# Kernel tuning notes

Hardware: AMD Instinct MI355X
Metric: run time of the kernel (lower is better)

## Reference

```python
import jax, jax.numpy as jnp
import numpy as np

VOCAB = 100000
EMB = 300
HID = 128


def setup_inputs() -> dict:
    key = jax.random.key(0)
    ks = jax.random.split(key, 12)
    inp = {
        "query_terms": jax.random.randint(ks[0], (32,), 0, VOCAB),
        "feedback_docs": jax.random.randint(ks[1], (128, 1024), 0, VOCAB),
        "n_terms": 10,
        "embedding": jax.random.normal(ks[2], (VOCAB, EMB), dtype=jnp.float32),
        # term_scorer: Linear(2*EMB -> HID), ReLU, Linear(HID -> 1), Sigmoid
        "sW1": jax.random.normal(ks[3], (2 * EMB, HID), dtype=jnp.float32) * 0.05,
        "sb1": jnp.zeros((HID,), dtype=jnp.float32),
        "sW2": jax.random.normal(ks[4], (HID, 1), dtype=jnp.float32) * 0.05,
        "sb2": jnp.zeros((1,), dtype=jnp.float32),
        # expansion_generator: Linear(3*EMB -> HID), ReLU, Linear(HID -> EMB)
        "eW1": jax.random.normal(ks[5], (3 * EMB, HID), dtype=jnp.float32) * 0.05,
        "eb1": jnp.zeros((HID,), dtype=jnp.float32),
        "eW2": jax.random.normal(ks[6], (HID, EMB), dtype=jnp.float32) * 0.05,
        "eb2": jnp.zeros((EMB,), dtype=jnp.float32),
    }
    return inp


def reference(query_terms, feedback_docs, n_terms, embedding,
              sW1, sb1, sW2, sb2, eW1, eb1, eW2, eb2):
    # query context: mean of query term embeddings  [EMB]
    query_ctx = embedding[query_terms].mean(axis=0)

    # gather all feedback-doc term embeddings, flatten docs  [N, EMB]
    flat_ids = feedback_docs.reshape(-1)
    term_emb = embedding[flat_ids]

    # per-term MLP score: sigmoid(W2 relu(W1 [term; query_ctx] + b1) + b2)
    x = jnp.concatenate(
        [term_emb, jnp.broadcast_to(query_ctx, term_emb.shape)], axis=-1)  # [N, 2*EMB]
    h = jax.nn.relu(x @ sW1 + sb1)
    scores = jax.nn.sigmoid(h @ sW2 + sb2)[:, 0]  # [N]

    # scatter-add scores by vocab id (replaces the defaultdict loop)
    weights = jax.ops.segment_sum(scores, flat_ids, num_segments=VOCAB)  # [VOCAB]

    # top-n_terms vocab ids by accumulated weight (unseen ids have weight 0)
    top_w, top_ids = jax.lax.top_k(weights, n_terms)

    # expansion embedding mean and generator MLP
    exp_mean = embedding[top_ids].mean(axis=0)  # [EMB]
    feat = jnp.concatenate([query_ctx, exp_mean, query_ctx * exp_mean])  # [3*EMB]
    expanded_query = jax.nn.relu(feat @ eW1 + eb1) @ eW2 + eb2  # [EMB]

    return expanded_query, top_ids, top_w
```

## Files before the change

### kernel.cpp

```cpp
#include <hip/hip_runtime.h>
#include <math.h>

#define VOCABN 100000
#define EMBD 300
#define HID 128
#define NQ 32
#define NTOP 10

#define NCHS 19
#define CMIN 3
#define NBLK_AC 1024
#define RANGE 98
#define RANGE_PAD 128
#define HB 512
#define KSLC 57

typedef __attribute__((ext_vector_type(8))) short bf16x8;
typedef __attribute__((ext_vector_type(4))) float f32x4;
typedef __attribute__((ext_vector_type(16))) float f32x16;
typedef __attribute__((ext_vector_type(4))) unsigned int u32x4;
typedef unsigned long long u64;

#define WS_HACC   400000
#define WS_QCTX   400512
#define WS_QCB    401712
#define WS_WFH    402224
#define WS_WFL    484144
#define WS_TPACK  566064

__device__ __forceinline__ void split8(const f32x4 a, const f32x4 b,
                                       u32x4* hi, u32x4* lo) {
    float ef[8] = {a.x, a.y, a.z, a.w, b.x, b.y, b.z, b.w};
    unsigned int hw[8], lw[8];
#pragma unroll
    for (int j = 0; j < 8; ++j) {
        unsigned int u = __float_as_uint(ef[j]);
        hw[j] = u >> 16;
        float r = __uint_as_float(u & 0xffff0000u);
        lw[j] = __float_as_uint(ef[j] - r) >> 16;
    }
    *hi = (u32x4){hw[0] | (hw[1] << 16), hw[2] | (hw[3] << 16),
                  hw[4] | (hw[5] << 16), hw[6] | (hw[7] << 16)};
    *lo = (u32x4){lw[0] | (lw[1] << 16), lw[2] | (lw[3] << 16),
                  lw[4] | (lw[5] << 16), lw[6] | (lw[7] << 16)};
}

__device__ __forceinline__ u64 packwi(float w, int id) {
    return ((u64)__float_as_uint(w) << 32) | (unsigned)(~id);
}

__device__ __forceinline__ void u64ins(u64* ms, int t, u64 v) {
    const int b = t * NTOP;
    if (v <= ms[b + NTOP - 1]) return;
    int p = NTOP - 1;
    while (p > 0 && v > ms[b + p - 1]) { ms[b + p] = ms[b + p - 1]; --p; }
    ms[b + p] = v;
}

#define LOADC_CORE(NN, S)                                                    \
    { int nn_ = (NN);                                                        \
      if (nn_ < NCHS) {                                                      \
          int k0_ = nn_ * 16 + khalf * 8;                                    \
          e0[S] = (k0_ + 4 <= EMBD) ? *(const f32x4*)(ebase + k0_) : zf4;    \
          e1[S] = (k0_ + 8 <= EMBD) ? *(const f32x4*)(ebase + k0_ + 4) : zf4;\
          _Pragma("unroll")                                                  \
          for (int t_ = 0; t_ < 4; ++t_) {                                   \
              long fo_ = ((long)(nn_ * 4 + t_) * 64 + lane) * 8;             \
              wh[S][t_] = *(const u32x4*)&wfH[fo_];                          \
              wl[S][t_] = *(const u32x4*)&wfL[fo_];                          \
          } } }

#define COMP_CORE(CC, S)                                                     \
    { if ((CC) < NCHS) {                                                     \
          union { bf16x8 v; u32x4 u; } eh_, el_;                             \
          split8(e0[S], e1[S], &eh_.u, &el_.u);                              \
          _Pragma("unroll")                                                  \
          for (int t_ = 0; t_ < 4; ++t_) {                                   \
              union { bf16x8 v; u32x4 u; } bh_, bl_;                         \
              bh_.u = wh[S][t_]; bl_.u = wl[S][t_];                          \
              acc[t_] = __builtin_amdgcn_mfma_f32_32x32x16_bf16(eh_.v, bh_.v, acc[t_], 0, 0, 0); \
              acc[t_] = __builtin_amdgcn_mfma_f32_32x32x16_bf16(eh_.v, bl_.v, acc[t_], 0, 0, 0); \
              acc[t_] = __builtin_amdgcn_mfma_f32_32x32x16_bf16(el_.v, bh_.v, acc[t_], 0, 0, 0); \
          } } }

#define SCORE_BATCH_BODY                                                     \
    {                                                                        \
        f32x16 acc[4];                                                       \
        _Pragma("unroll")                                                    \
        for (int t_ = 0; t_ < 4; ++t_)                                       \
            _Pragma("unroll")                                                \
            for (int r_ = 0; r_ < 16; ++r_) acc[t_][r_] = 0.f;               \
        f32x4 e0[2], e1[2];                                                  \
        u32x4 wh[2][4], wl[2][4];                                            \
        const f32x4 zf4 = (f32x4){0.f, 0.f, 0.f, 0.f};                       \
        LOADC_CORE(0, 0) LOADC_CORE(1, 1)                                    \
        for (int g_ = 0; g_ < 10; ++g_) {                                    \
            const int c_ = g_ * 2;                                           \
            COMP_CORE(c_ + 0, 0) LOADC_CORE(c_ + 2, 0)                       \
            COMP_CORE(c_ + 1, 1) LOADC_CORE(c_ + 3, 1)                       \
        }                                                                    \
        float pr[16];                                                        \
        _Pragma("unroll")                                                    \
        for (int r_ = 0; r_ < 16; ++r_) {                                    \
            float s_ = 0.f;                                                  \
            _Pragma("unroll")                                                \
            for (int t_ = 0; t_ < 4; ++t_) {                                 \
                float h_ = fmaxf(acc[t_][r_] + qv[t_], 0.f);                 \
                s_ += h_ * w2v[t_];                                          \
            }                                                                \
            s_ += __shfl_xor(s_, 1); s_ += __shfl_xor(s_, 2);                \
            s_ += __shfl_xor(s_, 4); s_ += __shfl_xor(s_, 8);                \
            s_ += __shfl_xor(s_, 16);                                        \
            pr[r_] = s_;                                                     \
        }                                                                    \
        if (lrow == 0) {                                                     \
            _Pragma("unroll")                                                \
            for (int r_ = 0; r_ < 16; ++r_)                                  \
                pv[(r_ & 3) + 8 * (r_ >> 2) + 4 * khalf] = pr[r_];           \
        }                                                                    \
        asm volatile("s_waitcnt lgkmcnt(0)" ::: "memory");                   \
        __builtin_amdgcn_sched_barrier(0);                                   \
    }

__global__ __launch_bounds__(256) void k_zero(int* __restrict__ p) {
    const int NI = (WS_HACC + 512) / 4;
    for (int i = blockIdx.x * 256 + threadIdx.x; i < NI; i += gridDim.x * 256)
        p[i] = 0;
}

__global__ __launch_bounds__(256) void k_histplus(
        const int* __restrict__ fdocs, int n, int* __restrict__ counts,
        const int* __restrict__ qterms, const float* __restrict__ emb,
        const float* __restrict__ sW1, const float* __restrict__ sb1,
        float* __restrict__ qctx, float* __restrict__ qcb,
        unsigned short* __restrict__ wfH, unsigned short* __restrict__ wfL) {
    const int b = blockIdx.x;
    const int t = threadIdx.x;
    if (b < HB) {
        for (int i = b * 256 + t; i < n; i += HB * 256)
            atomicAdd(&counts[fdocs[i]], 1);
        return;
    }
    if (b == HB) {
        __shared__ int qid[NQ];
        __shared__ float qc[EMBD];
        if (t < NQ) qid[t] = qterms[t];
        __syncthreads();
        for (int i = t; i < EMBD; i += 256) {
            float s = 0.f;
            for (int q = 0; q < NQ; ++q) s += emb[(long)qid[q] * EMBD + i];
            float v = s * (1.0f / NQ);
            qc[i] = v; qctx[i] = v;
        }
        __syncthreads();
        int col = t >> 1, half = t & 1;
        float a = 0.f;
        int k0 = half * 150;
        for (int k = k0; k < k0 + 150; ++k)
            a += qc[k] * sW1[(long)(EMBD + k) * HID + col];
        a += __shfl_xor(a, 1);
        if (half == 0) qcb[col] = a + sb1[col];
        return;
    }
    int i = (b - HB - 1) * 256 + t;
    int c = i >> 8;
    int rest = i & 255;
    int tile = rest >> 6;
    int l = rest & 63;
    int col = tile * 32 + (l & 31);
    int kbase = c * 16 + (l >> 5) * 8;
    unsigned int hw[8], lw[8];
#pragma unroll
    for (int j = 0; j < 8; ++j) {
        int k = kbase + j;
        unsigned int hi = 0, lo = 0;
        if (k < EMBD) {
            float f = sW1[(long)k * HID + col];
            unsigned int u = __float_as_uint(f);
            hi = u >> 16;
            float r = __uint_as_float(u & 0xffff0000u);
            lo = __float_as_uint(f - r) >> 16;
        }
        hw[j] = hi; lw[j] = lo;
    }
    long fo = ((long)(c * 4 + tile) * 64 + l) * 8;
    *(u32x4*)&wfH[fo] = (u32x4){hw[0] | (hw[1] << 16), hw[2] | (hw[3] << 16),
                                hw[4] | (hw[5] << 16), hw[6] | (hw[7] << 16)};
    *(u32x4*)&wfL[fo] = (u32x4){lw[0] | (lw[1] << 16), lw[2] | (lw[3] << 16),
                                lw[4] | (lw[5] << 16), lw[6] | (lw[7] << 16)};
}

__global__ __launch_bounds__(64) void k_scoreAC(
        const float* __restrict__ emb,
        const unsigned short* __restrict__ wfH,
        const unsigned short* __restrict__ wfL,
        const float* __restrict__ qcb,
        const float* __restrict__ sW2,
        const float* __restrict__ sb2,
        const int* __restrict__ counts,
        u64* __restrict__ tpack) {
    const int lane = threadIdx.x;
    const int blk = blockIdx.x;
    const int lrow = lane & 31;
    const int khalf = lane >> 5;
    const int base0 = blk * RANGE;

    __shared__ int   cl_id[RANGE_PAD];
    __shared__ int   cl_cnt[RANGE_PAD];
    __shared__ float allw[RANGE_PAD];
    __shared__ float pv[32];

    int ncl = 0;
#pragma unroll
    for (int it = 0; it < 2; ++it) {
        int i = it * 64 + lane;
        int v = base0 + i;
        int c = (i < RANGE && v < VOCABN) ? counts[v] : 0;
        bool pred = (c >= CMIN);
        u64 m = __ballot(pred);
        if (pred) {
            int pos = ncl + __popcll(m & ((1ull << lane) - 1ull));
            cl_id[pos] = v; cl_cnt[pos] = c;
        }
        ncl += __popcll(m);
    }
    __syncthreads();

    if (ncl == 0) {
        if (lane < NTOP) tpack[blk * NTOP + lane] = 0;
        return;
    }

    float qv[4], w2v[4];
#pragma unroll
    for (int t = 0; t < 4; ++t) {
        qv[t] = qcb[t * 32 + lrow];
        w2v[t] = sW2[t * 32 + lrow];
    }
    const float b2 = sb2[0];

    const int nb = (ncl + 31) >> 5;
    for (int bt = 0; bt < nb; ++bt) {
        int idx = bt * 32 + lrow;
        bool val = idx < ncl;
        int vrow = val ? cl_id[idx] : cl_id[0];
        const float* ebase = emb + (long)vrow * EMBD;

        SCORE_BATCH_BODY

        float w = -1.f;
        if (val) w = (float)cl_cnt[idx] / (1.f + expf(-(pv[lrow] + b2)));
        allw[bt * 32 + lrow] = w;
        __syncthreads();
    }

    for (int r = 0; r < NTOP; ++r) {
        float bw = -1.f; int bid = 0x7fffffff; int bslot = -1;
        for (int i = lane; i < ncl; i += 64) {
            float w = allw[i]; int id = cl_id[i];
            if (w > bw || (w == bw && id < bid)) { bw = w; bid = id; bslot = i; }
        }
#pragma unroll
        for (int mm = 1; mm < 64; mm <<= 1) {
            float ow = __shfl_xor(bw, mm);
            int oid = __shfl_xor(bid, mm);
            int osl = __shfl_xor(bslot, mm);
            if (ow > bw || (ow == bw && oid < bid)) { bw = ow; bid = oid; bslot = osl; }
        }
        if (lane == 0 && bslot >= 0) allw[bslot] = -2.f;
        if (lane == r) tpack[blk * NTOP + r] = (bw > 0.f) ? packwi(bw, bid) : 0;
        __syncthreads();
    }
}

__global__ __launch_bounds__(256) void k_mh(
        const u64* __restrict__ tpack,
        const float* __restrict__ qctx, const float* __restrict__ emb,
        const unsigned short* __restrict__ wfH, const unsigned short* __restrict__ wfL,
        const float* __restrict__ qcb, const float* __restrict__ sW2,
        const float* __restrict__ sb2, const int* __restrict__ counts,
        const float* __restrict__ eW1, const float* __restrict__ eb2,
        float* __restrict__ hacc, float* __restrict__ out) {
    __shared__ u64 ms[256 * NTOP];
    __shared__ int tid_s[NTOP];
    __shared__ float tw_s[NTOP];
    __shared__ float feat_s[KSLC + 7];
    __shared__ float pvs[4][32];
    const int t = threadIdx.x;
    const int b = blockIdx.x;

#pragma unroll
    for (int n = 0; n < NTOP; ++n) ms[t * NTOP + n] = 0;
    for (int i = t; i < NBLK_AC * NTOP; i += 256) u64ins(ms, t, tpack[i]);
    for (int s = 128; s > 0; s >>= 1) {
        __syncthreads();
        if (t < s) {
            const int ta = t * NTOP, tb = (t + s) * NTOP;
            u64 ov[NTOP]; int i = 0, j = 0;
#pragma unroll
            for (int n = 0; n < NTOP; ++n) {
                u64 va = ms[ta + i], vb = ms[tb + j];
                if (va > vb) { ov[n] = va; ++i; } else { ov[n] = vb; ++j; }
            }
#pragma unroll
            for (int n = 0; n < NTOP; ++n) ms[ta + n] = ov[n];
        }
    }
    __syncthreads();

    bool flag = (ms[NTOP - 1] != 0) &&
                (__uint_as_float((unsigned)(ms[NTOP - 1] >> 32)) >= 2.0f);

    if (!flag) {
        __syncthreads();
#pragma unroll
        for (int n = 0; n < NTOP; ++n) ms[t * NTOP + n] = 0;
        const int lane = t & 63;
        const int wave = t >> 6;
        const int lrow = lane & 31;
        const int khalf = lane >> 5;
        float qv[4], w2v[4];
#pragma unroll
        for (int tt = 0; tt < 4; ++tt) {
            qv[tt] = qcb[tt * 32 + lrow];
            w2v[tt] = sW2[tt * 32 + lrow];
        }
        const float b2 = sb2[0];
        const int ntile = (VOCABN + 31) / 32;
        for (int tile = wave; tile < ntile; tile += 4) {
            const int base = tile * 32;
            int rc = base + lrow; if (rc > VOCABN - 1) rc = VOCABN - 1;
            const float* ebase = emb + (long)rc * EMBD;
            float* pv = pvs[wave];
            SCORE_BATCH_BODY
            int gidx = base + lrow;
            if (khalf == 0 && gidx < VOCABN) {
                float w = (float)counts[gidx] / (1.f + expf(-(pv[lrow] + b2)));
                u64ins(ms, t, packwi(w, gidx));
            }
        }
        for (int s = 128; s > 0; s >>= 1) {
            __syncthreads();
            if (t < s) {
                const int ta = t * NTOP, tb = (t + s) * NTOP;
                u64 ov[NTOP]; int i = 0, j = 0;
#pragma unroll
                for (int n = 0; n < NTOP; ++n) {
                    u64 va = ms[ta + i], vb = ms[tb + j];
                    if (va > vb) { ov[n] = va; ++i; } else { ov[n] = vb; ++j; }
                }
#pragma unroll
                for (int n = 0; n < NTOP; ++n) ms[ta + n] = ov[n];
            }
        }
        __syncthreads();
    }

    if (t < NTOP) {
        u64 v = ms[t];
        int id = (int)(~(unsigned)v);
        if (id < 0 || id >= VOCABN) id = 0;
        tid_s[t] = id;
        tw_s[t] = (v == 0) ? -1.f : __uint_as_float((unsigned)(v >> 32));
    }
    __syncthreads();

    if (b == 16) {
        if (t < NTOP) {
            out[EMBD + t] = (float)tid_s[t];
            out[EMBD + NTOP + t] = tw_s[t];
        }
        for (int i = t; i < EMBD; i += 256) out[i] = eb2[i];
        return;
    }

    const int kstart = b * KSLC;
    const int kend = (kstart + KSLC < 3 * EMBD) ? kstart + KSLC : 3 * EMBD;
    const int klen = kend - kstart;
    for (int kk = t; kk < klen; kk += 256) {
        int k = kstart + kk;
        float f;
        if (k < EMBD) f = qctx[k];
        else {
            int d = (k < 2 * EMBD) ? k - EMBD : k - 2 * EMBD;
            float em_d = 0.f;
#pragma unroll
            for (int n = 0; n < NTOP; ++n) em_d += emb[(long)tid_s[n] * EMBD + d];
            em_d *= (1.0f / NTOP);
            f = (k < 2 * EMBD) ? em_d : qctx[d] * em_d;
        }
        feat_s[kk] = f;
    }
    __syncthreads();

    const int col = t & 127;
    const int kg = t >> 7;
    float a = 0.f;
    for (int k = kstart + kg; k < kend; k += 2)
        a += feat_s[k - kstart] * eW1[(long)k * HID + col];
    atomicAdd(&hacc[col], a);
}

__global__ __launch_bounds__(256) void k_out(
        const float* __restrict__ hacc, const float* __restrict__ eb1,
        const float* __restrict__ eW2, float* __restrict__ out) {
    const int b = blockIdx.x;
    const int t = threadIdx.x;
    __shared__ float hj[8];
    if (t < 8) {
        int j = b * 8 + t;
        hj[t] = fmaxf(hacc[j] + eb1[j], 0.f);
    }
    __syncthreads();
    for (int i = t; i < EMBD; i += 256) {
        float a = 0.f;
#pragma unroll
        for (int jj = 0; jj < 8; ++jj)
            a += hj[jj] * eW2[(long)(b * 8 + jj) * EMBD + i];
        atomicAdd(&out[i], a);
    }
}

extern "C" void kernel_launch(void* const* d_in, const int* in_sizes, int n_in,
                              void* d_out, int out_size, void* d_ws, size_t ws_size,
                              hipStream_t stream) {
    const int* qterms  = (const int*)d_in[0];
    const int* fdocs   = (const int*)d_in[1];
    const float* emb   = (const float*)d_in[3];
    const float* sW1   = (const float*)d_in[4];
    const float* sb1   = (const float*)d_in[5];
    const float* sW2   = (const float*)d_in[6];
    const float* sb2   = (const float*)d_in[7];
    const float* eW1   = (const float*)d_in[8];
    const float* eb1   = (const float*)d_in[9];
    const float* eW2   = (const float*)d_in[10];
    const float* eb2   = (const float*)d_in[11];
    char* ws = (char*)d_ws;
    float* out = (float*)d_out;

    int*   counts = (int*)ws;
    float* hacc   = (float*)(ws + WS_HACC);
    float* qctx   = (float*)(ws + WS_QCTX);
    float* qcb    = (float*)(ws + WS_QCB);
    unsigned short* wfH = (unsigned short*)(ws + WS_WFH);
    unsigned short* wfL = (unsigned short*)(ws + WS_WFL);
    u64*   tpack  = (u64*)(ws + WS_TPACK);

    int nflat = in_sizes[1];

    k_zero<<<512, 256, 0, stream>>>(counts);
    k_histplus<<<HB + 1 + 20, 256, 0, stream>>>(fdocs, nflat, counts, qterms, emb,
                                                sW1, sb1, qctx, qcb, wfH, wfL);
    k_scoreAC<<<NBLK_AC, 64, 0, stream>>>(emb, wfH, wfL, qcb, sW2, sb2, counts, tpack);
    k_mh<<<17, 256, 0, stream>>>(tpack, qctx, emb, wfH, wfL, qcb, sW2, sb2,
                                 counts, eW1, eb2, hacc, out);
    k_out<<<16, 256, 0, stream>>>(hacc, eb1, eW2, out);
}
```

Measured before the change: 84.59 us.

## Fuse expansion MLP into final kernel and replace zero kernel with memset

Merges the k_mh and k_out kernels into one k_final2 kernel. Each of 16 blocks now redundantly computes the full hidden layer (900x128 matvec) and then its own 19-element slice of the output, which removes the global hacc atomics, the hacc zeroing and one kernel launch. The custom zeroing kernel is replaced by hipMemsetAsync on the counts buffer. The cost is that every block reads all of eW1 and does the full first-layer matvec serially (450 iterations per thread), which lengthens the critical path of that stage.

Result: slower. 92.08 us (+8.9%).

```diff
diff --git a/kernel.cpp b/kernel.cpp
--- a/kernel.cpp
+++ b/kernel.cpp
@@ -13,7 +13,7 @@
 #define RANGE 98
 #define RANGE_PAD 128
 #define HB 512
-#define KSLC 57
+#define ISLC 19
 
 typedef __attribute__((ext_vector_type(8))) short bf16x8;
 typedef __attribute__((ext_vector_type(4))) float f32x4;
@@ -21,12 +21,11 @@
 typedef __attribute__((ext_vector_type(4))) unsigned int u32x4;
 typedef unsigned long long u64;
 
-#define WS_HACC   400000
-#define WS_QCTX   400512
-#define WS_QCB    401712
-#define WS_WFH    402224
-#define WS_WFL    484144
-#define WS_TPACK  566064
+#define WS_QCTX   400064
+#define WS_QCB    401280
+#define WS_WFH    401920
+#define WS_WFL    483840
+#define WS_TPACK  565760
 
 __device__ __forceinline__ void split8(const f32x4 a, const f32x4 b,
                                        u32x4* hi, u32x4* lo) {
@@ -122,12 +121,6 @@
         __builtin_amdgcn_sched_barrier(0);                                   \
     }
 
-__global__ __launch_bounds__(256) void k_zero(int* __restrict__ p) {
-    const int NI = (WS_HACC + 512) / 4;
-    for (int i = blockIdx.x * 256 + threadIdx.x; i < NI; i += gridDim.x * 256)
-        p[i] = 0;
-}
-
 __global__ __launch_bounds__(256) void k_histplus(
         const int* __restrict__ fdocs, int n, int* __restrict__ counts,
         const int* __restrict__ qterms, const float* __restrict__ emb,
@@ -273,18 +266,21 @@
     }
 }
 
-__global__ __launch_bounds__(256) void k_mh(
+__global__ __launch_bounds__(256) void k_final2(
         const u64* __restrict__ tpack,
         const float* __restrict__ qctx, const float* __restrict__ emb,
         const unsigned short* __restrict__ wfH, const unsigned short* __restrict__ wfL,
         const float* __restrict__ qcb, const float* __restrict__ sW2,
         const float* __restrict__ sb2, const int* __restrict__ counts,
-        const float* __restrict__ eW1, const float* __restrict__ eb2,
-        float* __restrict__ hacc, float* __restrict__ out) {
+        const float* __restrict__ eW1, const float* __restrict__ eb1,
+        const float* __restrict__ eW2, const float* __restrict__ eb2,
+        float* __restrict__ out) {
     __shared__ u64 ms[256 * NTOP];
     __shared__ int tid_s[NTOP];
     __shared__ float tw_s[NTOP];
-    __shared__ float feat_s[KSLC + 7];
+    __shared__ float feat_s[3 * EMBD];
+    __shared__ float hbuf[HID];
+    __shared__ float outv[ISLC];
     __shared__ float pvs[4][32];
     const int t = threadIdx.x;
     const int b = blockIdx.x;
@@ -370,55 +366,51 @@
             out[EMBD + t] = (float)tid_s[t];
             out[EMBD + NTOP + t] = tw_s[t];
         }
-        for (int i = t; i < EMBD; i += 256) out[i] = eb2[i];
         return;
     }
 
-    const int kstart = b * KSLC;
-    const int kend = (kstart + KSLC < 3 * EMBD) ? kstart + KSLC : 3 * EMBD;
-    const int klen = kend - kstart;
-    for (int kk = t; kk < klen; kk += 256) {
-        int k = kstart + kk;
-        float f;
-        if (k < EMBD) f = qctx[k];
-        else {
-            int d = (k < 2 * EMBD) ? k - EMBD : k - 2 * EMBD;
-            float em_d = 0.f;
-#pragma unroll
-            for (int n = 0; n < NTOP; ++n) em_d += emb[(long)tid_s[n] * EMBD + d];
-            em_d *= (1.0f / NTOP);
-            f = (k < 2 * EMBD) ? em_d : qctx[d] * em_d;
-        }
-        feat_s[kk] = f;
-    }
-    __syncthreads();
-
-    const int col = t & 127;
-    const int kg = t >> 7;
-    float a = 0.f;
-    for (int k = kstart + kg; k < kend; k += 2)
-        a += feat_s[k - kstart] * eW1[(long)k * HID + col];
-    atomicAdd(&hacc[col], a);
-}
-
-__global__ __launch_bounds__(256) void k_out(
-        const float* __restrict__ hacc, const float* __restrict__ eb1,
-        const float* __restrict__ eW2, float* __restrict__ out) {
-    const int b = blockIdx.x;
-    const int t = threadIdx.x;
-    __shared__ float hj[8];
-    if (t < 8) {
-        int j = b * 8 + t;
-        hj[t] = fmaxf(hacc[j] + eb1[j], 0.f);
-    }
-    __syncthreads();
-    for (int i = t; i < EMBD; i += 256) {
+    for (int d = t; d < EMBD; d += 256) {
+        float em_d = 0.f;
+#pragma unroll
+        for (int n = 0; n < NTOP; ++n) em_d += emb[(long)tid_s[n] * EMBD + d];
+        em_d *= (1.0f / NTOP);
+        float q = qctx[d];
+        feat_s[d] = q;
+        feat_s[EMBD + d] = em_d;
+        feat_s[2 * EMBD + d] = q * em_d;
+    }
+    __syncthreads();
+
+    {
+        int col = t >> 1, half = t & 1;
         float a = 0.f;
-#pragma unroll
-        for (int jj = 0; jj < 8; ++jj)
-            a += hj[jj] * eW2[(long)(b * 8 + jj) * EMBD + i];
-        atomicAdd(&out[i], a);
-    }
+        int k0 = half * 450;
+        for (int k = k0; k < k0 + 450; ++k)
+            a += feat_s[k] * eW1[(long)k * HID + col];
+        a += __shfl_xor(a, 1);
+        if (half == 0) hbuf[col] = fmaxf(a + eb1[col], 0.f);
+    }
+    if (t < ISLC) outv[t] = 0.f;
+    __syncthreads();
+
+    const int i0 = b * ISLC;
+    if (t < 8 * ISLC) {
+        int ii = t % ISLC;
+        int jg = t / ISLC;
+        int i = i0 + ii;
+        if (i < EMBD) {
+            float a = 0.f;
+#pragma unroll
+            for (int jj = 0; jj < 16; ++jj) {
+                int j = jg * 16 + jj;
+                a += hbuf[j] * eW2[(long)j * EMBD + i];
+            }
+            atomicAdd(&outv[ii], a);
+        }
+    }
+    __syncthreads();
+    if (t < ISLC && i0 + t < EMBD)
+        out[i0 + t] = eb2[i0 + t] + outv[t];
 }
 
 extern "C" void kernel_launch(void* const* d_in, const int* in_sizes, int n_in,
@@ -439,7 +431,6 @@
     float* out = (float*)d_out;
 
     int*   counts = (int*)ws;
-    float* hacc   = (float*)(ws + WS_HACC);
     float* qctx   = (float*)(ws + WS_QCTX);
     float* qcb    = (float*)(ws + WS_QCB);
     unsigned short* wfH = (unsigned short*)(ws + WS_WFH);
@@ -448,11 +439,10 @@
 
     int nflat = in_sizes[1];
 
-    k_zero<<<512, 256, 0, stream>>>(counts);
+    hipMemsetAsync(counts, 0, VOCABN * sizeof(int), stream);
     k_histplus<<<HB + 1 + 20, 256, 0, stream>>>(fdocs, nflat, counts, qterms, emb,
                                                 sW1, sb1, qctx, qcb, wfH, wfL);
     k_scoreAC<<<NBLK_AC, 64, 0, stream>>>(emb, wfH, wfL, qcb, sW2, sb2, counts, tpack);
-    k_mh<<<17, 256, 0, stream>>>(tpack, qctx, emb, wfH, wfL, qcb, sW2, sb2,
-                                 counts, eW1, eb2, hacc, out);
-    k_out<<<16, 256, 0, stream>>>(hacc, eb1, eW2, out);
-}
+    k_final2<<<17, 256, 0, stream>>>(tpack, qctx, emb, wfH, wfL, qcb, sW2, sb2,
+                                     counts, eW1, eb1, eW2, eb2, out);
+}
```

## Replace global atomic histogram and zero kernel with LDS vocab-sliced histogram

Applied to the files above, without the earlier changes.

Removes the separate zeroing kernel and the global-atomic histogram. The vocab is split into 64 slices, and each block builds its slice's counts in LDS atomics, then writes them directly to global memory, so no prior zeroing is needed. The qctx block now zeroes hacc. This saves one kernel launch and the global atomic contention, but each of the 64 blocks must read all 131k doc ids, multiplying global reads of fdocs.

Result: slower. 151.4 us (+79.0%).

```diff
diff --git a/kernel.cpp b/kernel.cpp
--- a/kernel.cpp
+++ b/kernel.cpp
@@ -12,7 +12,8 @@
 #define NBLK_AC 1024
 #define RANGE 98
 #define RANGE_PAD 128
-#define HB 512
+#define HSB 64
+#define HSLICE 1563
 #define KSLC 57
 
 typedef __attribute__((ext_vector_type(8))) short bf16x8;
@@ -122,29 +123,35 @@
         __builtin_amdgcn_sched_barrier(0);                                   \
     }
 
-__global__ __launch_bounds__(256) void k_zero(int* __restrict__ p) {
-    const int NI = (WS_HACC + 512) / 4;
-    for (int i = blockIdx.x * 256 + threadIdx.x; i < NI; i += gridDim.x * 256)
-        p[i] = 0;
-}
-
-__global__ __launch_bounds__(256) void k_histplus(
+__global__ __launch_bounds__(256) void k_pre(
         const int* __restrict__ fdocs, int n, int* __restrict__ counts,
         const int* __restrict__ qterms, const float* __restrict__ emb,
         const float* __restrict__ sW1, const float* __restrict__ sb1,
-        float* __restrict__ qctx, float* __restrict__ qcb,
+        float* __restrict__ qctx, float* __restrict__ qcb, float* __restrict__ hacc,
         unsigned short* __restrict__ wfH, unsigned short* __restrict__ wfL) {
     const int b = blockIdx.x;
     const int t = threadIdx.x;
-    if (b < HB) {
-        for (int i = b * 256 + t; i < n; i += HB * 256)
-            atomicAdd(&counts[fdocs[i]], 1);
+    if (b < HSB) {
+        __shared__ int hl[HSLICE];
+        const int lo = b * HSLICE;
+        for (int i = t; i < HSLICE; i += 256) hl[i] = 0;
+        __syncthreads();
+        for (int i = t; i < n; i += 256) {
+            int rel = fdocs[i] - lo;
+            if ((unsigned)rel < (unsigned)HSLICE) atomicAdd(&hl[rel], 1);
+        }
+        __syncthreads();
+        for (int i = t; i < HSLICE; i += 256) {
+            int v = lo + i;
+            if (v < VOCABN) counts[v] = hl[i];
+        }
         return;
     }
-    if (b == HB) {
+    if (b == HSB) {
         __shared__ int qid[NQ];
         __shared__ float qc[EMBD];
         if (t < NQ) qid[t] = qterms[t];
+        if (t < HID) hacc[t] = 0.f;
         __syncthreads();
         for (int i = t; i < EMBD; i += 256) {
             float s = 0.f;
@@ -162,7 +169,7 @@
         if (half == 0) qcb[col] = a + sb1[col];
         return;
     }
-    int i = (b - HB - 1) * 256 + t;
+    int i = (b - HSB - 1) * 256 + t;
     int c = i >> 8;
     int rest = i & 255;
     int tile = rest >> 6;
@@ -173,15 +180,15 @@
 #pragma unroll
     for (int j = 0; j < 8; ++j) {
         int k = kbase + j;
-        unsigned int hi = 0, lo = 0;
+        unsigned int hi = 0, lo2 = 0;
         if (k < EMBD) {
             float f = sW1[(long)k * HID + col];
             unsigned int u = __float_as_uint(f);
             hi = u >> 16;
             float r = __uint_as_float(u & 0xffff0000u);
-            lo = __float_as_uint(f - r) >> 16;
-        }
-        hw[j] = hi; lw[j] = lo;
+            lo2 = __float_as_uint(f - r) >> 16;
+        }
+        hw[j] = hi; lw[j] = lo2;
     }
     long fo = ((long)(c * 4 + tile) * 64 + l) * 8;
     *(u32x4*)&wfH[fo] = (u32x4){hw[0] | (hw[1] << 16), hw[2] | (hw[3] << 16),
@@ -448,9 +455,8 @@
 
     int nflat = in_sizes[1];
 
-    k_zero<<<512, 256, 0, stream>>>(counts);
-    k_histplus<<<HB + 1 + 20, 256, 0, stream>>>(fdocs, nflat, counts, qterms, emb,
-                                                sW1, sb1, qctx, qcb, wfH, wfL);
+    k_pre<<<HSB + 1 + 20, 256, 0, stream>>>(fdocs, nflat, counts, qterms, emb,
+                                            sW1, sb1, qctx, qcb, hacc, wfH, wfL);
     k_scoreAC<<<NBLK_AC, 64, 0, stream>>>(emb, wfH, wfL, qcb, sW2, sb2, counts, tpack);
     k_mh<<<17, 256, 0, stream>>>(tpack, qctx, emb, wfH, wfL, qcb, sW2, sb2,
                                  counts, eW1, eb2, hacc, out);
```
